# Kernel tuning notes

Measured on AMD Instinct MI355X. Metric: run time of the kernel, lower is better.

The kernel has to match this reference:

```python
import jax, jax.numpy as jnp
import numpy as np
import math

H = 512      # d_model
N = 64       # d_state
B = 16
L = 4096
DT_MIN, DT_MAX = 0.001, 0.1


def setup_inputs() -> dict:
    key = jax.random.key(0)
    ks = jax.random.split(key, 6)
    u = jax.random.normal(ks[0], (B, H, L), dtype=jnp.float32)
    # S4DKernel parameters
    C = jax.random.normal(ks[1], (H, N // 2, 2), dtype=jnp.float32)  # view_as_real of cfloat C
    log_dt = (jax.random.uniform(ks[2], (H,), dtype=jnp.float32)
              * (math.log(DT_MAX) - math.log(DT_MIN)) + math.log(DT_MIN))
    log_A_real = jnp.log(0.5 * jnp.ones((H, N // 2), dtype=jnp.float32))
    A_imag = math.pi * jnp.broadcast_to(jnp.arange(N // 2, dtype=jnp.float32), (H, N // 2))
    # S4D parameters
    D = jax.random.normal(ks[3], (H,), dtype=jnp.float32)
    # output_linear: Conv1d(H, 2H, kernel_size=1) -> weight (2H, H), bias (2H,)
    W = jax.random.normal(ks[4], (2 * H, H), dtype=jnp.float32) * (1.0 / math.sqrt(H))
    b = jax.random.normal(ks[5], (2 * H,), dtype=jnp.float32) * 0.01
    return {"u": u, "C": C, "log_dt": log_dt, "log_A_real": log_A_real,
            "A_imag": A_imag, "D": D, "W": W, "b": b}


def _s4d_kernel(C, log_dt, log_A_real, A_imag, L):
    """Generate the (H, L) convolution kernel from diagonal SSM parameters."""
    dt = jnp.exp(log_dt)                                    # (H,)
    Cc = C[..., 0] + 1j * C[..., 1]                         # (H, N/2) complex
    A = -jnp.exp(log_A_real) + 1j * A_imag                  # (H, N/2)
    dtA = A * dt[:, None]                                   # (H, N/2)
    # Vandermonde: exp(dtA * l) for l in [0, L)
    K = jnp.exp(dtA[:, :, None] * jnp.arange(L, dtype=jnp.float32))  # (H, N/2, L)
    Cw = Cc * (jnp.exp(dtA) - 1.0) / A                      # (H, N/2)
    k = 2.0 * jnp.einsum('hn,hnl->hl', Cw, K).real          # (H, L)
    return k


def reference(u, C, log_dt, log_A_real, A_imag, D, W, b):
    Lc = u.shape[-1]
    k = _s4d_kernel(C, log_dt, log_A_real, A_imag, Lc)      # (H, L)
    # FFT long convolution (linear conv via zero-padding to 2L)
    k_f = jnp.fft.rfft(k, n=2 * Lc)                          # (H, L+1)
    u_f = jnp.fft.rfft(u, n=2 * Lc)                          # (B, H, L+1)
    y = jnp.fft.irfft(u_f * k_f, n=2 * Lc)[..., :Lc]         # (B, H, L)
    y = y + u * D[:, None]
    y = jax.nn.gelu(y, approximate=False)                    # torch nn.GELU default
    # output_linear: 1x1 Conv1d (H -> 2H) then GLU over channel dim
    z = jnp.einsum('oh,bhl->bol', W, y) + b[None, :, None]   # (B, 2H, L)
    a, g = jnp.split(z, 2, axis=1)
    return a * jax.nn.sigmoid(g)                             # (B, H, L)
```

## Files before the change

### kernel.cpp

```cpp
#include <hip/hip_runtime.h>

#define BB 16
#define HH 512
#define NH 32
#define LL 4096
#define TCH 64
#define NCH 64
#define KA 128

static_assert(TCH * NCH == LL, "chunking");

typedef __attribute__((ext_vector_type(8))) short bf16x8;
typedef __attribute__((ext_vector_type(4))) float f32x4;

static __device__ __forceinline__ unsigned short f2bf(float x) {
    return __builtin_bit_cast(unsigned short, (__bf16)x);
}
static __device__ __forceinline__ float bf2f(unsigned short b) {
    return __builtin_bit_cast(float, ((unsigned)b) << 16);
}
static __device__ __forceinline__ unsigned pack2(float a, float b) {
    return (unsigned)f2bf(a) | ((unsigned)f2bf(b) << 16);
}
static __device__ __forceinline__ float gelu1(float x) {
    float a = fmaf(0.071354816f * x, x * x, 1.5957691f * x);
    return x * __builtin_amdgcn_rcpf(1.0f + __expf(-a));
}
static __device__ __forceinline__ unsigned gelu_pk(unsigned p) {
    float a = gelu1(bf2f((unsigned short)(p & 0xffffu)));
    float b = gelu1(bf2f((unsigned short)(p >> 16)));
    return pack2(a, b);
}

static __device__ __forceinline__ void gload_lds16(const void* g, void* l) {
#if __has_builtin(__builtin_amdgcn_global_load_lds)
    __builtin_amdgcn_global_load_lds(
        (const __attribute__((address_space(1))) unsigned int*)g,
        (__attribute__((address_space(3))) unsigned int*)l, 16, 0, 0);
#else
    *(uint4*)l = *(const uint4*)g;
#endif
}

__global__ void k0_params(const float* __restrict__ C,
                          const float* __restrict__ log_dt,
                          const float* __restrict__ lAr,
                          const float* __restrict__ Aim,
                          float* __restrict__ c2R,  float* __restrict__ c2I,
                          float* __restrict__ ltR,  float* __restrict__ ltI,
                          float* __restrict__ xrA,  float* __restrict__ xiA)
{
    int tid = blockIdx.x * 256 + threadIdx.x;
    if (tid >= HH * NH) return;
    int h = tid >> 5;
    float dt = expf(log_dt[h]);
    float Ar = -expf(lAr[tid]);
    float Ai = Aim[tid];
    float xr = Ar * dt, xi = Ai * dt;
    xrA[tid] = xr; xiA[tid] = xi;
    float er = expf(xr);
    float lr = er * cosf(xi);
    float li = er * sinf(xi);
    float wr = lr - 1.0f, wi = li;
    float inv = 1.0f / (Ar * Ar + Ai * Ai);
    float qr = (wr * Ar + wi * Ai) * inv;
    float qi = (wi * Ar - wr * Ai) * inv;
    float cr = C[2 * tid], ci = C[2 * tid + 1];
    c2R[tid] =  2.0f * (cr * qr - ci * qi);
    c2I[tid] = -2.0f * (cr * qi + ci * qr);
    float eT = expf((float)TCH * xr);
    float aT = (float)TCH * xi;
    ltR[tid] = eT * cosf(aT);
    ltI[tid] = eT * sinf(aT);
}

__global__ void kw_pack(const float* __restrict__ W, const float* __restrict__ bias,
                        unsigned short* __restrict__ Wp, float* __restrict__ bp)
{
    int tid = blockIdx.x * 256 + threadIdx.x;
    int drow = tid >> 6;
    int kc = (tid & 63) * 8;
    int src = (drow & 1) ? (drow >> 1) + HH : (drow >> 1);
    const float4* s = (const float4*)(W + (size_t)src * HH + kc);
    float4 a = s[0], b4 = s[1];
    uint4 pack;
    pack.x = pack2(a.x, a.y);
    pack.y = pack2(a.z, a.w);
    pack.z = pack2(b4.x, b4.y);
    pack.w = pack2(b4.z, b4.w);
    *(uint4*)(Wp + (size_t)drow * HH + kc) = pack;
    if (tid < 2 * HH)
        bp[tid] = bias[(tid & 1) ? (tid >> 1) + HH : (tid >> 1)];
}

__global__ __launch_bounds__(64) void kA_build(
    const float* __restrict__ c2R, const float* __restrict__ c2I,
    const float* __restrict__ xrA, const float* __restrict__ xiA,
    const float* __restrict__ Dv,
    unsigned short* __restrict__ Apan, unsigned short* __restrict__ Vpan)
{
    int h = blockIdx.x;
    int t = threadIdx.x;
    __shared__ float s_xr[NH], s_xi[NH], s_cr[NH], s_ci[NH], s_k[TCH];
    if (t < NH) {
        s_xr[t] = xrA[h * NH + t]; s_xi[t] = xiA[h * NH + t];
        s_cr[t] = c2R[h * NH + t]; s_ci[t] = c2I[h * NH + t];
    }
    __syncthreads();
    {
        float d = (float)t;
        float acc = 0.f;
#pragma unroll
        for (int n = 0; n < NH; ++n) {
            float er = __expf(s_xr[n] * d);
            float sv, cv; __sincosf(s_xi[n] * d, &sv, &cv);
            acc = fmaf(s_cr[n], er * cv, fmaf(s_ci[n], er * sv, acc));
        }
        s_k[t] = acc;
    }
    __syncthreads();
    float k0d = s_k[0] + Dv[h];
    unsigned short row[KA];
#pragma unroll
    for (int tau = 0; tau < TCH; ++tau)
        row[tau] = f2bf((tau < t) ? s_k[t - tau] : (tau == t ? k0d : 0.f));
    float tp = (float)(t + 1);
#pragma unroll
    for (int n = 0; n < NH; ++n) {
        float er = __expf(s_xr[n] * tp);
        float sv, cv; __sincosf(s_xi[n] * tp, &sv, &cv);
        float pr = er * cv, pi = er * sv;
        row[TCH + 2 * n]     = f2bf(fmaf(s_cr[n], pr,  s_ci[n] * pi));
        row[TCH + 2 * n + 1] = f2bf(fmaf(s_ci[n], pr, -s_cr[n] * pi));
    }
    {
        uint4* dst = (uint4*)(Apan + ((size_t)h * TCH + t) * KA);
        const uint4* src = (const uint4*)row;
#pragma unroll
        for (int i = 0; i < 16; ++i) dst[i] = src[i];
    }
    {
        int n = t >> 1, cm = t & 1;
        float xr = s_xr[n], xi = s_xi[n];
        unsigned short vrow[TCH];
#pragma unroll
        for (int tau = 0; tau < TCH; ++tau) {
            float p = (float)(TCH - 1 - tau);
            float er = __expf(xr * p);
            float sv, cv; __sincosf(xi * p, &sv, &cv);
            vrow[tau] = f2bf(cm ? er * sv : er * cv);
        }
        uint4* vd = (uint4*)(Vpan + ((size_t)h * TCH + t) * TCH);
        const uint4* vs = (const uint4*)vrow;
#pragma unroll
        for (int i = 0; i < 8; ++i) vd[i] = vs[i];
    }
}

__global__ __launch_bounds__(256)
__attribute__((amdgpu_waves_per_eu(2)))
void kBCD(
    const float* __restrict__ u,
    const unsigned short* __restrict__ Apan, const unsigned short* __restrict__ Vpan,
    const float* __restrict__ ltR, const float* __restrict__ ltI,
    unsigned short* __restrict__ yb)
{
    __shared__ unsigned short Sl[4][TCH * TCH];
    int h = blockIdx.x & (HH - 1), g = blockIdx.x >> 9;
    int tid = threadIdx.x;
    int lane = tid & 63, w = tid >> 6;
    int b = g * 4 + w;
    int lrow = lane & 15, hi = lane >> 4, lk8 = hi * 8;
    const float* ug = u + ((size_t)b * HH + h) * LL;
    const unsigned short* Ap = Apan + (size_t)h * TCH * KA;
    const unsigned short* Vp = Vpan + (size_t)h * TCH * TCH;
    char* Sw = (char*)Sl[w];

    bf16x8 ub[2][4];
#pragma unroll
    for (int ks = 0; ks < 2; ++ks)
#pragma unroll
        for (int n = 0; n < 4; ++n) {
            int c = n * 16 + lrow;
            const float* up = ug + c * TCH + ks * 32 + lk8;
            float4 f0 = *(const float4*)up, f1 = *(const float4*)(up + 4);
            bf16x8 v;
            v[0]=f2bf(f0.x); v[1]=f2bf(f0.y); v[2]=f2bf(f0.z); v[3]=f2bf(f0.w);
            v[4]=f2bf(f1.x); v[5]=f2bf(f1.y); v[6]=f2bf(f1.z); v[7]=f2bf(f1.w);
            ub[ks][n] = v;
        }

#pragma unroll
    for (int m = 0; m < 4; ++m) {
        f32x4 accE[4];
#pragma unroll
        for (int n = 0; n < 4; ++n) { f32x4 z = {0.f,0.f,0.f,0.f}; accE[n] = z; }
#pragma unroll
        for (int ks = 0; ks < 2; ++ks) {
            bf16x8 vf = *(const bf16x8*)(Vp + (m * 16 + lrow) * TCH + ks * 32 + lk8);
#pragma unroll
            for (int n = 0; n < 4; ++n)
                accE[n] = __builtin_amdgcn_mfma_f32_16x16x32_bf16(vf, ub[ks][n], accE[n], 0, 0, 0);
        }
        int j0 = m * 16 + hi * 4;
#pragma unroll
        for (int n = 0; n < 4; ++n) {
            int c = n * 16 + lrow;
            uint2 p; p.x = pack2(accE[n][0], accE[n][1]); p.y = pack2(accE[n][2], accE[n][3]);
            *(uint2*)(Sw + c * 128 + ((2 * j0) ^ ((c & 7) << 4))) = p;
        }
    }
    asm volatile("s_waitcnt lgkmcnt(0)" ::: "memory");

    if (lane < NH) {
        int n = lane;
        float ar = ltR[h * NH + n], ai = ltI[h * NH + n];
        float sr = 0.f, si = 0.f;
#pragma unroll
        for (int gg = 0; gg < 8; ++gg) {
            unsigned ev[8];
#pragma unroll
            for (int k = 0; k < 8; ++k)
                ev[k] = *(const unsigned*)(Sw + (gg * 8 + k) * 128 + ((4 * n) ^ (k << 4)));
#pragma unroll
            for (int k = 0; k < 8; ++k) {
                *(unsigned*)(Sw + (gg * 8 + k) * 128 + ((4 * n) ^ (k << 4))) = pack2(sr, si);
                float er = bf2f((unsigned short)(ev[k] & 0xffffu));
                float ei = bf2f((unsigned short)(ev[k] >> 16));
                float nsr = fmaf(ar, sr, fmaf(-ai, si, er));
                float nsi = fmaf(ar, si, fmaf(ai, sr, ei));
                sr = nsr; si = nsi;
            }
        }
    }
    asm volatile("s_waitcnt lgkmcnt(0)" ::: "memory");

    bf16x8 sfr[2][4];
#pragma unroll
    for (int ks = 0; ks < 2; ++ks)
#pragma unroll
        for (int n = 0; n < 4; ++n) {
            int c = n * 16 + lrow;
            sfr[ks][n] = *(const bf16x8*)(Sw + c * 128 + ((ks * 64 + lk8 * 2) ^ ((c & 7) << 4)));
        }

    uint2 yp[4][4];
#pragma unroll
    for (int m = 0; m < 4; ++m) {
        f32x4 acc[4];
#pragma unroll
        for (int n = 0; n < 4; ++n) { f32x4 z = {0.f,0.f,0.f,0.f}; acc[n] = z; }
#pragma unroll
        for (int ks = 0; ks < 2; ++ks) {
            bf16x8 af = *(const bf16x8*)(Ap + (m * 16 + lrow) * KA + ks * 32 + lk8);
#pragma unroll
            for (int n = 0; n < 4; ++n)
                acc[n] = __builtin_amdgcn_mfma_f32_16x16x32_bf16(af, ub[ks][n], acc[n], 0, 0, 0);
        }
#pragma unroll
        for (int ks = 0; ks < 2; ++ks) {
            bf16x8 af = *(const bf16x8*)(Ap + (m * 16 + lrow) * KA + 64 + ks * 32 + lk8);
#pragma unroll
            for (int n = 0; n < 4; ++n)
                acc[n] = __builtin_amdgcn_mfma_f32_16x16x32_bf16(af, sfr[ks][n], acc[n], 0, 0, 0);
        }
#pragma unroll
        for (int n = 0; n < 4; ++n) {
            yp[m][n].x = pack2(acc[n][0], acc[n][1]);
            yp[m][n].y = pack2(acc[n][2], acc[n][3]);
        }
    }
    asm volatile("s_waitcnt lgkmcnt(0)" ::: "memory");

#pragma unroll
    for (int m = 0; m < 4; ++m) {
        int t0b = m * 32 + hi * 8;
#pragma unroll
        for (int n = 0; n < 4; ++n) {
            int c = n * 16 + lrow;
            *(uint2*)(Sw + c * 128 + (t0b ^ ((c & 7) << 4))) = yp[m][n];
        }
    }
    asm volatile("s_waitcnt lgkmcnt(0)" ::: "memory");
    unsigned short* yrow = yb + ((size_t)b * HH + h) * LL;
#pragma unroll
    for (int it = 0; it < 8; ++it) {
        int o = it * 1024 + lane * 16;
        int c = o >> 7;
        int sl = o & 127;
        uint4 v = *(const uint4*)(Sw + c * 128 + (sl ^ ((c & 7) << 4)));
        *(uint4*)((char*)yrow + o) = v;
    }
}

__global__ __launch_bounds__(256) void kT_transpose(
    const unsigned short* __restrict__ yb, unsigned short* __restrict__ yt)
{
    __shared__ unsigned short T[64][130];
    int bid = blockIdx.x;
    int lt = bid & 31;
    int ht = (bid >> 5) & 7;
    int b  = bid >> 8;
    int t = threadIdx.x;
#pragma unroll
    for (int r = 0; r < 4; ++r) {
        int chunk = r * 256 + t;
        int row = chunk >> 4;
        int c16 = chunk & 15;
        uint4 v = *(const uint4*)(yb + ((size_t)(b * HH + ht * 64 + row)) * LL
                                     + lt * 128 + c16 * 8);
        v.x = gelu_pk(v.x); v.y = gelu_pk(v.y);
        v.z = gelu_pk(v.z); v.w = gelu_pk(v.w);
        *(uint4*)&T[row][c16 * 8] = v;
    }
    __syncthreads();
    int oct = t & 7, lgrp = t >> 3;
    size_t obase = ((size_t)b * LL + (size_t)lt * 128) * HH + ht * 64 + oct * 8;
#pragma unroll
    for (int r = 0; r < 2; ++r) {
        int l = (r * 32 + lgrp) * 2;
        unsigned v[8];
#pragma unroll
        for (int k = 0; k < 8; ++k)
            v[k] = *(const unsigned*)&T[oct * 8 + k][l];
        uint4 w0, w1;
        w0.x = (v[0] & 0xffffu) | (v[1] << 16);
        w0.y = (v[2] & 0xffffu) | (v[3] << 16);
        w0.z = (v[4] & 0xffffu) | (v[5] << 16);
        w0.w = (v[6] & 0xffffu) | (v[7] << 16);
        w1.x = (v[0] >> 16) | (v[1] & 0xffff0000u);
        w1.y = (v[2] >> 16) | (v[3] & 0xffff0000u);
        w1.z = (v[4] >> 16) | (v[5] & 0xffff0000u);
        w1.w = (v[6] >> 16) | (v[7] & 0xffff0000u);
        *(uint4*)(yt + obase + (size_t)l * HH) = w0;
        *(uint4*)(yt + obase + (size_t)(l + 1) * HH) = w1;
    }
}

#define NKT4 8

__global__ __launch_bounds__(512, 2) void k4_gemm(
    const unsigned short* __restrict__ Wp, const float* __restrict__ bp,
    const unsigned short* __restrict__ yt, float* __restrict__ out)
{
    __shared__ unsigned short As4[2][256 * 64];
    __shared__ unsigned short Bs4[2][256 * 64];
    int tid = threadIdx.x;
    int bidx = (blockIdx.x & 7) * 128 + (blockIdx.x >> 3);
    int mtile = bidx & 3, ntile = bidx >> 2;
    int mbase = mtile * 256, nbase = ntile * 256;
    int lane = tid & 63;
    int wv = tid >> 6;
    int wr = wv >> 2, wc = wv & 3;
    int lrow = lane & 15;
    int hi = lane >> 4;
    int rx = (lrow & 7) << 4;

#define STAGE4(kt, buf) do {                                                   \
    _Pragma("unroll")                                                          \
    for (int rr = 0; rr < 4; ++rr) {                                           \
        int _r = rr * 64 + (tid >> 3);                                         \
        int _u = (tid & 7) ^ (_r & 7);                                         \
        gload_lds16(Wp + (size_t)(mbase + _r) * HH + (kt) * 64 + _u * 8,       \
                    &As4[buf][_r * 64 + (tid & 7) * 8]);                       \
        gload_lds16(yt + (size_t)(nbase + _r) * HH + (kt) * 64 + _u * 8,       \
                    &Bs4[buf][_r * 64 + (tid & 7) * 8]);                       \
    }                                                                          \
} while (0)

    f32x4 acc[8][4];
#pragma unroll
    for (int m = 0; m < 8; ++m)
#pragma unroll
        for (int n = 0; n < 4; ++n) { f32x4 z = {0.f,0.f,0.f,0.f}; acc[m][n] = z; }

    STAGE4(0, 0);
    STAGE4(1, 1);
    asm volatile("s_waitcnt vmcnt(8)" ::: "memory");
    asm volatile("s_barrier" ::: "memory");

#pragma unroll 1
    for (int kt = 0; kt < NKT4; ++kt) {
        int cur = kt & 1;
        const char* Ab = (const char*)&As4[cur][0];
        const char* Bb = (const char*)&Bs4[cur][0];
        bf16x8 bfr[4][2];
#pragma unroll
        for (int n = 0; n < 4; ++n) {
            int R = wc * 64 + n * 16 + lrow;
#pragma unroll
            for (int ks = 0; ks < 2; ++ks)
                bfr[n][ks] = *(const bf16x8*)(Bb + R * 128 + ((ks * 64 + hi * 16) ^ rx));
        }
#pragma unroll
        for (int q = 0; q < 4; ++q) {
            bf16x8 af[2][2];
#pragma unroll
            for (int mi = 0; mi < 2; ++mi) {
                int R = wr * 128 + (q * 2 + mi) * 16 + lrow;
#pragma unroll
                for (int ks = 0; ks < 2; ++ks)
                    af[mi][ks] = *(const bf16x8*)(Ab + R * 128 + ((ks * 64 + hi * 16) ^ rx));
            }
#pragma unroll
            for (int mi = 0; mi < 2; ++mi)
#pragma unroll
                for (int n = 0; n < 4; ++n)
#pragma unroll
                    for (int ks = 0; ks < 2; ++ks)
                        acc[q * 2 + mi][n] = __builtin_amdgcn_mfma_f32_16x16x32_bf16(
                            af[mi][ks], bfr[n][ks], acc[q * 2 + mi][n], 0, 0, 0);
        }
        asm volatile("s_barrier" ::: "memory");
        if (kt + 2 < NKT4) {
            STAGE4(kt + 2, cur);
            asm volatile("s_waitcnt vmcnt(8)" ::: "memory");
        } else {
            asm volatile("s_waitcnt vmcnt(0)" ::: "memory");
        }
        asm volatile("s_barrier" ::: "memory");
    }
#undef STAGE4

#pragma unroll
    for (int m = 0; m < 8; ++m) {
        int go = mbase + wr * 128 + m * 16 + hi * 4;
        float4 bv = *(const float4*)(bp + go);
#pragma unroll
        for (int nf = 0; nf < 4; ++nf) {
            int col  = nbase + wc * 64 + nf * 16 + lrow;
            int bcol = col >> 12;
            int lcol = col & (LL - 1);
            f32x4 v = acc[m][nf];
            float a0 = v[0] + bv.x, g0 = v[1] + bv.y;
            float a1 = v[2] + bv.z, g1 = v[3] + bv.w;
            float o0 = a0 / (1.0f + __expf(-g0));
            float o1 = a1 / (1.0f + __expf(-g1));
            size_t ob = ((size_t)bcol * HH + (size_t)(go >> 1)) * LL + lcol;
            out[ob] = o0;
            out[ob + LL] = o1;
        }
    }
}

extern "C" void kernel_launch(void* const* d_in, const int* in_sizes, int n_in,
                              void* d_out, int out_size, void* d_ws, size_t ws_size,
                              hipStream_t stream) {
    const float* u    = (const float*)d_in[0];
    const float* C    = (const float*)d_in[1];
    const float* ldt  = (const float*)d_in[2];
    const float* lar  = (const float*)d_in[3];
    const float* aim  = (const float*)d_in[4];
    const float* Dv   = (const float*)d_in[5];
    const float* W    = (const float*)d_in[6];
    const float* bias = (const float*)d_in[7];
    float* out = (float*)d_out;

    char* w = (char*)d_ws;
    float* c2R = (float*)w; w += (size_t)HH * NH * 4;
    float* c2I = (float*)w; w += (size_t)HH * NH * 4;
    float* ltR = (float*)w; w += (size_t)HH * NH * 4;
    float* ltI = (float*)w; w += (size_t)HH * NH * 4;
    float* xrA = (float*)w; w += (size_t)HH * NH * 4;
    float* xiA = (float*)w; w += (size_t)HH * NH * 4;
    float* bp  = (float*)w; w += (size_t)2 * HH * 4;
    unsigned short* Wp   = (unsigned short*)w; w += (size_t)2 * HH * HH * 2;
    unsigned short* Apan = (unsigned short*)w; w += (size_t)HH * TCH * KA * 2;
    unsigned short* Vpan = (unsigned short*)w; w += (size_t)HH * TCH * TCH * 2;
    unsigned short* yt   = (unsigned short*)w; w += (size_t)BB * LL * HH * 2;

    unsigned short* yb = (unsigned short*)d_out;

    k0_params   <<<dim3(64),   dim3(256), 0, stream>>>(C, ldt, lar, aim, c2R, c2I, ltR, ltI, xrA, xiA);
    kw_pack     <<<dim3(256),  dim3(256), 0, stream>>>(W, bias, Wp, bp);
    kA_build    <<<dim3(512),  dim3(64),  0, stream>>>(c2R, c2I, xrA, xiA, Dv, Apan, Vpan);
    kBCD        <<<dim3(2048), dim3(256), 0, stream>>>(u, Apan, Vpan, ltR, ltI, yb);
    kT_transpose<<<dim3(4096), dim3(256), 0, stream>>>(yb, yt);
    k4_gemm     <<<dim3(1024), dim3(512), 0, stream>>>(Wp, bp, yt, out);
}
```

Measured before the change: 178.2 us.

## Restructure GEMM mainloop into 4-stage BK=32 pipeline with split phases

Replaces the double-buffered BK=64 GEMM loop with a 4-buffer, BK=32 ring that prefetches three k-tiles ahead. Each iteration is split into two half-phases: one loads the A fragments and issues the A global stage, the other loads the remaining A fragments and issues the B stage. MFMA bursts are bracketed by barriers and priority raises so loads interleave with compute. The LDS swizzle is rewritten for the 64-byte rows. This adds more barriers per k-step and a more intricate vmcnt accounting in exchange for deeper latency hiding.

```diff
diff --git a/kernel.cpp b/kernel.cpp
--- a/kernel.cpp
+++ b/kernel.cpp
@@ -337,14 +337,15 @@
     }
 }
 
-#define NKT4 8
+#define BK4 32
+#define NKT4 16
 
 __global__ __launch_bounds__(512, 2) void k4_gemm(
     const unsigned short* __restrict__ Wp, const float* __restrict__ bp,
     const unsigned short* __restrict__ yt, float* __restrict__ out)
 {
-    __shared__ unsigned short As4[2][256 * 64];
-    __shared__ unsigned short Bs4[2][256 * 64];
+    __shared__ unsigned short As4[4][256 * BK4];
+    __shared__ unsigned short Bs4[4][256 * BK4];
     int tid = threadIdx.x;
     int bidx = (blockIdx.x & 7) * 128 + (blockIdx.x >> 3);
     int mtile = bidx & 3, ntile = bidx >> 2;
@@ -354,19 +355,21 @@
     int wr = wv >> 2, wc = wv & 3;
     int lrow = lane & 15;
     int hi = lane >> 4;
-    int rx = (lrow & 7) << 4;
-
-#define STAGE4(kt, buf) do {                                                   \
-    _Pragma("unroll")                                                          \
-    for (int rr = 0; rr < 4; ++rr) {                                           \
-        int _r = rr * 64 + (tid >> 3);                                         \
-        int _u = (tid & 7) ^ (_r & 7);                                         \
-        gload_lds16(Wp + (size_t)(mbase + _r) * HH + (kt) * 64 + _u * 8,       \
-                    &As4[buf][_r * 64 + (tid & 7) * 8]);                       \
-        gload_lds16(yt + (size_t)(nbase + _r) * HH + (kt) * 64 + _u * 8,       \
-                    &Bs4[buf][_r * 64 + (tid & 7) * 8]);                       \
-    }                                                                          \
-} while (0)
+
+#define STGA(kt) do { _Pragma("unroll") for (int _j = 0; _j < 2; ++_j) {       \
+        int _c = wv * 2 + _j;                                                  \
+        int _r = _c * 16 + (lane >> 2);                                        \
+        int _u = (lane & 3) ^ ((_r >> 1) & 3);                                 \
+        gload_lds16(Wp + (size_t)(mbase + _r) * HH + (kt) * BK4 + _u * 8,      \
+                    (char*)&As4[(kt) & 3][0] + _c * 1024 + lane * 16);         \
+    } } while (0)
+#define STGB(kt) do { _Pragma("unroll") for (int _j = 0; _j < 2; ++_j) {       \
+        int _c = wv * 2 + _j;                                                  \
+        int _r = _c * 16 + (lane >> 2);                                        \
+        int _u = (lane & 3) ^ ((_r >> 1) & 3);                                 \
+        gload_lds16(yt + (size_t)(nbase + _r) * HH + (kt) * BK4 + _u * 8,      \
+                    (char*)&Bs4[(kt) & 3][0] + _c * 1024 + lane * 16);         \
+    } } while (0)
 
     f32x4 acc[8][4];
 #pragma unroll
@@ -374,53 +377,60 @@
 #pragma unroll
         for (int n = 0; n < 4; ++n) { f32x4 z = {0.f,0.f,0.f,0.f}; acc[m][n] = z; }
 
-    STAGE4(0, 0);
-    STAGE4(1, 1);
+    STGA(0); STGB(0); STGA(1); STGB(1); STGA(2); STGB(2);
     asm volatile("s_waitcnt vmcnt(8)" ::: "memory");
     asm volatile("s_barrier" ::: "memory");
 
 #pragma unroll 1
     for (int kt = 0; kt < NKT4; ++kt) {
-        int cur = kt & 1;
-        const char* Ab = (const char*)&As4[cur][0];
-        const char* Bb = (const char*)&Bs4[cur][0];
-        bf16x8 bfr[4][2];
+        const char* Ab = (const char*)&As4[kt & 3][0];
+        const char* Bb = (const char*)&Bs4[kt & 3][0];
+        bf16x8 bfr[4], af[4];
 #pragma unroll
         for (int n = 0; n < 4; ++n) {
             int R = wc * 64 + n * 16 + lrow;
-#pragma unroll
-            for (int ks = 0; ks < 2; ++ks)
-                bfr[n][ks] = *(const bf16x8*)(Bb + R * 128 + ((ks * 64 + hi * 16) ^ rx));
-        }
-#pragma unroll
-        for (int q = 0; q < 4; ++q) {
-            bf16x8 af[2][2];
-#pragma unroll
-            for (int mi = 0; mi < 2; ++mi) {
-                int R = wr * 128 + (q * 2 + mi) * 16 + lrow;
-#pragma unroll
-                for (int ks = 0; ks < 2; ++ks)
-                    af[mi][ks] = *(const bf16x8*)(Ab + R * 128 + ((ks * 64 + hi * 16) ^ rx));
-            }
-#pragma unroll
-            for (int mi = 0; mi < 2; ++mi)
-#pragma unroll
-                for (int n = 0; n < 4; ++n)
-#pragma unroll
-                    for (int ks = 0; ks < 2; ++ks)
-                        acc[q * 2 + mi][n] = __builtin_amdgcn_mfma_f32_16x16x32_bf16(
-                            af[mi][ks], bfr[n][ks], acc[q * 2 + mi][n], 0, 0, 0);
-        }
+            bfr[n] = *(const bf16x8*)(Bb + R * 64 + ((hi ^ ((R >> 1) & 3)) << 4));
+        }
+#pragma unroll
+        for (int mi = 0; mi < 4; ++mi) {
+            int R = wr * 128 + mi * 16 + lrow;
+            af[mi] = *(const bf16x8*)(Ab + R * 64 + ((hi ^ ((R >> 1) & 3)) << 4));
+        }
+        if (kt + 3 < NKT4) STGA(kt + 3);
         asm volatile("s_barrier" ::: "memory");
-        if (kt + 2 < NKT4) {
-            STAGE4(kt + 2, cur);
-            asm volatile("s_waitcnt vmcnt(8)" ::: "memory");
-        } else {
-            asm volatile("s_waitcnt vmcnt(0)" ::: "memory");
-        }
+        asm volatile("s_waitcnt lgkmcnt(0)" ::: "memory");
+        __builtin_amdgcn_sched_barrier(0);
+        __builtin_amdgcn_s_setprio(1);
+#pragma unroll
+        for (int mi = 0; mi < 4; ++mi)
+#pragma unroll
+            for (int n = 0; n < 4; ++n)
+                acc[mi][n] = __builtin_amdgcn_mfma_f32_16x16x32_bf16(af[mi], bfr[n], acc[mi][n], 0, 0, 0);
+        __builtin_amdgcn_s_setprio(0);
         asm volatile("s_barrier" ::: "memory");
-    }
-#undef STAGE4
+#pragma unroll
+        for (int mi = 0; mi < 4; ++mi) {
+            int R = wr * 128 + (4 + mi) * 16 + lrow;
+            af[mi] = *(const bf16x8*)(Ab + R * 64 + ((hi ^ ((R >> 1) & 3)) << 4));
+        }
+        if (kt + 3 < NKT4) STGB(kt + 3);
+        if (kt + 3 < NKT4)           asm volatile("s_waitcnt vmcnt(8)" ::: "memory");
+        else if (kt == NKT4 - 3)     asm volatile("s_waitcnt vmcnt(4)" ::: "memory");
+        else if (kt == NKT4 - 2)     asm volatile("s_waitcnt vmcnt(0)" ::: "memory");
+        asm volatile("s_barrier" ::: "memory");
+        asm volatile("s_waitcnt lgkmcnt(0)" ::: "memory");
+        __builtin_amdgcn_sched_barrier(0);
+        __builtin_amdgcn_s_setprio(1);
+#pragma unroll
+        for (int mi = 0; mi < 4; ++mi)
+#pragma unroll
+            for (int n = 0; n < 4; ++n)
+                acc[4 + mi][n] = __builtin_amdgcn_mfma_f32_16x16x32_bf16(af[mi], bfr[n], acc[4 + mi][n], 0, 0, 0);
+        __builtin_amdgcn_s_setprio(0);
+        asm volatile("s_barrier" ::: "memory");
+    }
+#undef STGA
+#undef STGB
 
 #pragma unroll
     for (int m = 0; m < 8; ++m) {
```

After: 182.9 us. +2.6%, slower.
